# Kernel tuning notes

Hardware: AMD Instinct MI355X
Metric: run time of the kernel (lower is better)

## Reference

```python
import jax, jax.numpy as jnp
import numpy as np
import math

B, S, D, H = 2, 2048, 1024, 16
DH = D // H  # head_dim = 64


def setup_inputs() -> dict:
    key = jax.random.key(0)
    k0, k1, k2 = jax.random.split(key, 3)
    x = jax.random.normal(k0, (B, S, D), dtype=jnp.float32)
    Wi = jax.random.normal(k1, (3 * D, D), dtype=jnp.float32) * 0.02  # torch (out,in) layout
    bi = jnp.zeros((3 * D,), dtype=jnp.float32)
    Wo = jax.random.normal(k2, (D, D), dtype=jnp.float32) * 0.02
    bo = jnp.zeros((D,), dtype=jnp.float32)
    return {"x": x, "Wi": Wi, "bi": bi, "Wo": Wo, "bo": bo, "causal_mask": 1}


def reference(x, Wi, bi, Wo, bo, causal_mask):
    b, s, d = x.shape
    # fused QKV projection: nn.Linear applies x @ W.T + b
    qkv = x @ Wi.T + bi                      # (b, s, 3d)
    q, k, v = jnp.split(qkv, 3, axis=-1)
    # (b, s, d) -> (b, h, s, dh)
    def to_heads(t):
        return t.reshape(b, s, H, DH).transpose(0, 2, 1, 3)
    q, k, v = to_heads(q), to_heads(k), to_heads(v)
    scores = jnp.einsum("bhqd,bhkd->bhqk", q, k)  # (b, h, s, s)
    if causal_mask:
        # mask strictly-upper triangle with -inf BEFORE scaling (as in source; -inf unaffected)
        tri = jnp.triu(jnp.ones((s, s), dtype=bool), k=1)
        scores = jnp.where(tri, -jnp.inf, scores)
    scores = scores / math.sqrt(DH)
    weight = jax.nn.softmax(scores, axis=-1)
    out = jnp.einsum("bhqk,bhkd->bhqd", weight, v)  # (b, h, s, dh)
    out = out.transpose(0, 2, 1, 3).reshape(b, s, d)
    return out @ Wo.T + bo
```

## Files before the change

kernel.cpp:

```cpp
#include <hip/hip_runtime.h>
#include <hip/hip_bf16.h>
#include <stdint.h>

#define B_    2
#define S_    2048
#define D_    1024
#define H_    16
#define DH_   64
#define MTOT  (B_*S_)
#define NQKV  (3*D_)

typedef __attribute__((ext_vector_type(8))) short  bf16x8;
typedef __attribute__((ext_vector_type(4))) short  bf16x4;
typedef __attribute__((ext_vector_type(4))) float  f32x4;
typedef __attribute__((ext_vector_type(8))) unsigned short u16x8;
typedef unsigned short ushort_t;

__device__ __forceinline__ ushort_t f2bf(float f) {
  union { float f; unsigned int i; } v; v.f = f;
  unsigned int r = v.i + 0x7FFF + ((v.i >> 16) & 1);
  return (ushort_t)(r >> 16);
}

__device__ __forceinline__ unsigned cvt_pk_bf16(float lo, float hi) {
  unsigned r;
  asm("v_cvt_pk_bf16_f32 %0, %1, %2" : "=v"(r) : "v"(lo), "v"(hi));
  return r;
}

__device__ __forceinline__ float fexp2(float x) {
  float r;
  asm("v_exp_f32 %0, %1" : "=v"(r) : "v"(x));
  return r;
}

#if __has_builtin(__builtin_amdgcn_mfma_f32_16x16x16_bf16)
__device__ __forceinline__ f32x4 mfma16(bf16x4 a, bf16x4 b, f32x4 c) {
  return __builtin_amdgcn_mfma_f32_16x16x16_bf16(a, b, c, 0, 0, 0);
}
#elif __has_builtin(__builtin_amdgcn_mfma_f32_16x16x16bf16_1k)
__device__ __forceinline__ f32x4 mfma16(bf16x4 a, bf16x4 b, f32x4 c) {
  return __builtin_amdgcn_mfma_f32_16x16x16bf16_1k(a, b, c, 0, 0, 0);
}
#else
__device__ __forceinline__ f32x4 mfma16(bf16x4 a, bf16x4 b, f32x4 c) {
  asm volatile("v_mfma_f32_16x16x16_bf16 %0, %1, %2, %0"
               : "+v"(c) : "v"(a), "v"(b));
  return c;
}
#endif

__device__ __forceinline__ void gl_lds16(const ushort_t* g, ushort_t* l) {
  __builtin_amdgcn_global_load_lds(
      (const __attribute__((address_space(1))) unsigned int*)g,
      (__attribute__((address_space(3))) unsigned int*)l, 16, 0, 0);
}

#define CVN1 (MTOT*D_/8)
#define CVN2 (NQKV*D_/8)
#define CVN3 (D_*D_/8)
__global__ __launch_bounds__(256) void cvt_all(
    const float* __restrict__ x, const float* __restrict__ Wi, const float* __restrict__ Wo,
    ushort_t* __restrict__ xb, ushort_t* __restrict__ Wib, ushort_t* __restrict__ Wob) {
  int i = blockIdx.x * blockDim.x + threadIdx.x;
  const float* src; ushort_t* dst; int k;
  if (i < CVN1)            { src = x;  dst = xb;  k = i; }
  else if (i < CVN1+CVN2)  { src = Wi; dst = Wib; k = i - CVN1; }
  else                     { src = Wo; dst = Wob; k = i - CVN1 - CVN2; }
  const float4* s4 = (const float4*)src;
  float4 a = s4[2*k], b = s4[2*k+1];
  u16x8 o;
  o[0]=f2bf(a.x); o[1]=f2bf(a.y); o[2]=f2bf(a.z); o[3]=f2bf(a.w);
  o[4]=f2bf(b.x); o[5]=f2bf(b.y); o[6]=f2bf(b.z); o[7]=f2bf(b.w);
  ((u16x8*)dst)[k] = o;
}

#define BKQ 32
#define BKO 64
#define QSCALE 0.18033688011112042f
__global__ __launch_bounds__(256) void gemm_qkv(
    const ushort_t* __restrict__ Abf, const ushort_t* __restrict__ Bbf,
    const float* __restrict__ bias,
    ushort_t* __restrict__ qb, ushort_t* __restrict__ kb, ushort_t* __restrict__ vb) {
  __shared__ __align__(16) ushort_t Al[128*BKQ];
  __shared__ __align__(16) ushort_t Bl[128*BKQ];
  int tid = threadIdx.x;
  int w = tid >> 6, lane = tid & 63;
  int wrow = (w >> 1) * 64, wcol = (w & 1) * 64;
  int m0 = blockIdx.y * 128, n0 = blockIdx.x * 128;
  const int K = D_;
  f32x4 zero = {0.f, 0.f, 0.f, 0.f};
  f32x4 acc[4][4];
  for (int i=0;i<4;i++) for (int j=0;j<4;j++) acc[i][j] = zero;

  for (int k0 = 0; k0 < K; k0 += BKQ) {
    __syncthreads();
    for (int it = 0; it < 2; ++it) {
      int c = it*256 + tid;
      int row = c >> 2, cc = c & 3;
      int lbase = (it*256 + w*64) * 8;
      gl_lds16(Abf + (size_t)(m0+row)*K + k0 + cc*8, Al + lbase);
      gl_lds16(Bbf + (size_t)(n0+row)*K + k0 + cc*8, Bl + lbase);
    }
    asm volatile("s_waitcnt vmcnt(0)" ::: "memory");
    __syncthreads();
    int kof = (lane >> 4) * 8;
    bf16x8 af[4], bfr[4];
    for (int i=0;i<4;i++) af[i]  = *(const bf16x8*)(Al + (wrow + i*16 + (lane&15))*BKQ + kof);
    for (int j=0;j<4;j++) bfr[j] = *(const bf16x8*)(Bl + (wcol + j*16 + (lane&15))*BKQ + kof);
    for (int i=0;i<4;i++)
      for (int j=0;j<4;j++)
        acc[i][j] = __builtin_amdgcn_mfma_f32_16x16x32_bf16(af[i], bfr[j], acc[i][j], 0, 0, 0);
  }
  for (int i=0;i<4;i++)
    for (int j=0;j<4;j++)
      for (int r=0;r<4;r++) {
        int gm = m0 + wrow + i*16 + (lane>>4)*4 + r;
        int gn = n0 + wcol + j*16 + (lane&15);
        float v = acc[i][j][r] + bias[gn];
        int b = gm >> 11, s = gm & (S_-1);
        int sect = gn >> 10, hn = gn & (D_-1);
        int hh = hn >> 6, d = hn & 63;
        size_t idx = (((size_t)(b*H_ + hh))*S_ + s)*DH_ + d;
        if (sect == 0) v *= QSCALE;
        ushort_t val = f2bf(v);
        if (sect == 0) qb[idx] = val;
        else if (sect == 1) kb[idx] = val;
        else vb[idx] = val;
      }
}

__global__ __launch_bounds__(256) void transpose_v(
    const ushort_t* __restrict__ vb, ushort_t* __restrict__ vtb) {
  __shared__ ushort_t T[64*72];
  int bh = blockIdx.y;
  int s0 = blockIdx.x * 64;
  int tid = threadIdx.x;
  const ushort_t* src = vb + (size_t)bh * S_ * DH_;
  ushort_t* dst = vtb + (size_t)bh * DH_ * S_;
  for (int it = 0; it < 2; ++it) {
    int c = it*256 + tid;
    int row = c >> 3, cc = c & 7;
    *(uint4*)&T[row*72 + cc*8] = *(const uint4*)(src + (size_t)(s0+row)*DH_ + cc*8);
  }
  __syncthreads();
  for (int it = 0; it < 2; ++it) {
    int c = it*256 + tid;
    int d = c >> 3, sc = c & 7;
    u16x8 o;
    #pragma unroll
    for (int e = 0; e < 8; ++e) o[e] = T[(sc*8+e)*72 + d];
    *(u16x8*)(dst + (size_t)d*S_ + s0 + sc*8) = o;
  }
}

#define KVB 64
#define DTHR 8.0f
__global__ __launch_bounds__(256) void attn_fwd(
    const ushort_t* __restrict__ qb, const ushort_t* __restrict__ kb,
    const ushort_t* __restrict__ vtb, ushort_t* __restrict__ attnb,
    const int* __restrict__ causal) {
  int wg = blockIdx.x;
  int xcd = wg & 7;
  int j = wg >> 3;
  int v = j >> 5;
  int u = j & 31;
  int a = u >> 2;
  int qi = v*8 + ((v & 1) ? (7 - a) : a);
  int qblk = 31 - qi;
  int bh = (u & 3) * 8 + xcd;
  int b = bh >> 4, h = bh & 15;
  int tid = threadIdx.x, w = tid >> 6, lane = tid & 63;
  int g = lane >> 4, q16 = lane & 15;
  const ushort_t* qh  = qb  + (size_t)bh * S_ * DH_;
  const ushort_t* kh  = kb  + (size_t)bh * S_ * DH_;
  const ushort_t* vth = vtb + (size_t)bh * DH_ * S_;
  __shared__ __align__(16) ushort_t Kl[2][KVB*64];
  __shared__ __align__(16) ushort_t Vtl[2][64*KVB];
  bool use_causal = (causal[0] != 0);

  int nkv = use_causal ? (qblk + 1) : (S_/KVB);
  int qw = qblk*64 + w*16;

  bf16x8 qc0 = *(const bf16x8*)(qh + (size_t)(qw + q16)*DH_ +  0 + g*8);
  bf16x8 qc1 = *(const bf16x8*)(qh + (size_t)(qw + q16)*DH_ + 32 + g*8);

  int c0 = tid, c1 = tid + 256;
  int r0 = c0 >> 3, sw0 = ((c0 & 7) ^ (r0 & 7)) * 8;
  int r1 = c1 >> 3, sw1 = ((c1 & 7) ^ (r1 & 7)) * 8;
  const ushort_t* kp0 = kh + r0*DH_ + sw0;
  const ushort_t* kp1 = kh + r1*DH_ + sw1;
  const ushort_t* vp0 = vth + (size_t)r0*S_ + sw0;
  const ushort_t* vp1 = vth + (size_t)r1*S_ + sw1;

  auto stage = [&](int t, int buf) {
    size_t kadv = (size_t)(t*KVB) * DH_;
    int vadv = t*KVB;
    gl_lds16(kp0 + kadv, &Kl[buf][c0*8]);
    gl_lds16(kp1 + kadv, &Kl[buf][c1*8]);
    gl_lds16(vp0 + vadv, &Vtl[buf][c0*8]);
    gl_lds16(vp1 + vadv, &Vtl[buf][c1*8]);
  };

  f32x4 zero = {0.f,0.f,0.f,0.f};
  f32x4 o[4];
  #pragma unroll
  for (int dt=0;dt<4;dt++) o[dt] = zero;
  float mrun = -1e30f, lrun = 0.f;

  stage(0, 0);
  asm volatile("s_waitcnt vmcnt(0)" ::: "memory");
  __builtin_amdgcn_s_barrier();

  for (int it = 0; it < nkv; ++it) {
    int cur = it & 1;
    int kvbase = it * KVB;
    if (it + 1 < nkv) stage(it + 1, cur ^ 1);

    f32x4 sacc[4];
    #pragma unroll
    for (int j2=0;j2<4;j2++) sacc[j2] = zero;
    #pragma unroll
    for (int kk=0;kk<2;kk++) {
      bf16x8 qf = kk ? qc1 : qc0;
      #pragma unroll
      for (int j2=0;j2<4;j2++) {
        int row = j2*16 + q16;
        int slot = (kk*4 + g) ^ (row & 7);
        bf16x8 kf = *(const bf16x8*)(&Kl[cur][row*64 + slot*8]);
        sacc[j2] = __builtin_amdgcn_mfma_f32_16x16x32_bf16(kf, qf, sacc[j2], 0, 0, 0);
      }
    }
    if (use_causal && kvbase + KVB - 1 > qw) {
      int qd = qw + q16 - kvbase;
      #pragma unroll
      for (int j2=0;j2<4;j2++)
        #pragma unroll
        for (int r=0;r<4;r++)
          if (16*j2 + 4*g + r > qd) sacc[j2][r] = -1e30f;
    }
    float m0v = fmaxf(fmaxf(sacc[0][0], sacc[0][1]), fmaxf(sacc[0][2], sacc[0][3]));
    float m1v = fmaxf(fmaxf(sacc[1][0], sacc[1][1]), fmaxf(sacc[1][2], sacc[1][3]));
    float m2v = fmaxf(fmaxf(sacc[2][0], sacc[2][1]), fmaxf(sacc[2][2], sacc[2][3]));
    float m3v = fmaxf(fmaxf(sacc[3][0], sacc[3][1]), fmaxf(sacc[3][2], sacc[3][3]));
    float mx = fmaxf(fmaxf(m0v, m1v), fmaxf(m2v, m3v));
    mx = fmaxf(mx, __shfl_xor(mx, 16, 64));
    mx = fmaxf(mx, __shfl_xor(mx, 32, 64));
    if (!__all(mx - mrun <= DTHR)) {
      float mnew = fmaxf(mrun, mx);
      float alpha = fexp2(mrun - mnew);
      lrun *= alpha;
      float av0 = __shfl(alpha, 4*g + 0, 64);
      float av1 = __shfl(alpha, 4*g + 1, 64);
      float av2 = __shfl(alpha, 4*g + 2, 64);
      float av3 = __shfl(alpha, 4*g + 3, 64);
      #pragma unroll
      for (int dt=0;dt<4;dt++) {
        o[dt][0] *= av0; o[dt][1] *= av1; o[dt][2] *= av2; o[dt][3] *= av3;
      }
      mrun = mnew;
    }
    float p[4][4];
    float rs = 0.f;
    #pragma unroll
    for (int j2=0;j2<4;j2++)
      #pragma unroll
      for (int r=0;r<4;r++) {
        p[j2][r] = fexp2(sacc[j2][r] - mrun);
        rs += p[j2][r];
      }
    rs += __shfl_xor(rs, 16, 64);
    rs += __shfl_xor(rs, 32, 64);
    lrun += rs;
    #pragma unroll
    for (int s=0;s<4;s++) {
      union { unsigned u2[2]; bf16x4 v2; } pk;
      pk.u2[0] = cvt_pk_bf16(p[s][0], p[s][1]);
      pk.u2[1] = cvt_pk_bf16(p[s][2], p[s][3]);
      int E = 16*s + 4*g;
      #pragma unroll
      for (int dt=0;dt<4;dt++) {
        int row = dt*16 + q16;
        int off = row*64 + ((E >> 3) ^ (row & 7))*8 + (E & 7);
        bf16x4 vf = *(const bf16x4*)(&Vtl[cur][off]);
        o[dt] = mfma16(pk.v2, vf, o[dt]);
      }
    }
    asm volatile("s_waitcnt vmcnt(0)" ::: "memory");
    __builtin_amdgcn_s_barrier();
  }
  float li0 = 1.f / __shfl(lrun, 4*g + 0, 64);
  float li1 = 1.f / __shfl(lrun, 4*g + 1, 64);
  float li2 = 1.f / __shfl(lrun, 4*g + 2, 64);
  float li3 = 1.f / __shfl(lrun, 4*g + 3, 64);
  #pragma unroll
  for (int r=0;r<4;r++) {
    float li = (r==0)?li0:(r==1)?li1:(r==2)?li2:li3;
    int q = qw + 4*g + r;
    #pragma unroll
    for (int dt=0;dt<4;dt++) {
      int d = dt*16 + q16;
      attnb[((size_t)(b*S_ + q))*D_ + h*DH_ + d] = f2bf(o[dt][r] * li);
    }
  }
}

__global__ __launch_bounds__(512) void gemm_out(
    const ushort_t* __restrict__ Abf, const ushort_t* __restrict__ Bbf,
    const float* __restrict__ bias, float* __restrict__ out) {
  __shared__ __align__(16) ushort_t Al[128*BKO];
  __shared__ __align__(16) ushort_t Bl[128*BKO];
  int tid = threadIdx.x;
  int w = tid >> 6, lane = tid & 63;
  int g = lane >> 4, q16 = lane & 15;
  int wrow = (w >> 2) * 64, wcol = (w & 3) * 32;
  int m0 = blockIdx.y * 128, n0 = blockIdx.x * 128;
  const int K = D_;
  f32x4 zero = {0.f,0.f,0.f,0.f};
  f32x4 acc[4][2];
  for (int i=0;i<4;i++) for (int j=0;j<2;j++) acc[i][j] = zero;

  for (int k0 = 0; k0 < K; k0 += BKO) {
    __syncthreads();
    #pragma unroll
    for (int it = 0; it < 2; ++it) {
      int c = it*512 + tid;
      int row = c >> 3, scc = ((c & 7) ^ (row & 7)) * 8;
      gl_lds16(Abf + (size_t)(m0+row)*K + k0 + scc, Al + c*8);
      gl_lds16(Bbf + (size_t)(n0+row)*K + k0 + scc, Bl + c*8);
    }
    asm volatile("s_waitcnt vmcnt(0)" ::: "memory");
    __syncthreads();
    #pragma unroll
    for (int kk = 0; kk < 2; ++kk) {
      bf16x8 af[4], bfr[2];
      #pragma unroll
      for (int i=0;i<4;i++) {
        int row = wrow + i*16 + q16;
        int slot = ((kk*4 + g) ^ (row & 7)) * 8;
        af[i] = *(const bf16x8*)(Al + row*BKO + slot);
      }
      #pragma unroll
      for (int j=0;j<2;j++) {
        int row = wcol + j*16 + q16;
        int slot = ((kk*4 + g) ^ (row & 7)) * 8;
        bfr[j] = *(const bf16x8*)(Bl + row*BKO + slot);
      }
      #pragma unroll
      for (int i=0;i<4;i++)
        #pragma unroll
        for (int j=0;j<2;j++)
          acc[i][j] = __builtin_amdgcn_mfma_f32_16x16x32_bf16(af[i], bfr[j], acc[i][j], 0, 0, 0);
    }
  }
  #pragma unroll
  for (int i=0;i<4;i++)
    #pragma unroll
    for (int j=0;j<2;j++)
      #pragma unroll
      for (int r=0;r<4;r++) {
        int gm = m0 + wrow + i*16 + g*4 + r;
        int gn = n0 + wcol + j*16 + q16;
        out[(size_t)gm*D_ + gn] = acc[i][j][r] + bias[gn];
      }
}

extern "C" void kernel_launch(void* const* d_in, const int* in_sizes, int n_in,
                              void* d_out, int out_size, void* d_ws, size_t ws_size,
                              hipStream_t stream) {
  const float* x  = (const float*)d_in[0];
  const float* Wi = (const float*)d_in[1];
  const float* bi = (const float*)d_in[2];
  const float* Wo = (const float*)d_in[3];
  const float* bo = (const float*)d_in[4];
  const int* causal = (const int*)d_in[5];
  float* out = (float*)d_out;

  ushort_t* xb   = (ushort_t*)d_ws;
  ushort_t* Wib  = xb  + (size_t)MTOT*D_;
  ushort_t* Wob  = Wib + (size_t)NQKV*D_;
  ushort_t* qbuf = Wob + (size_t)D_*D_;
  ushort_t* kbuf = qbuf + (size_t)B_*H_*S_*DH_;
  ushort_t* vbuf = kbuf + (size_t)B_*H_*S_*DH_;
  ushort_t* attnb = vbuf + (size_t)B_*H_*S_*DH_;
  ushort_t* vtb  = xb;

  int ntot = CVN1 + CVN2 + CVN3;
  cvt_all<<<(ntot+255)/256, 256, 0, stream>>>(x, Wi, Wo, xb, Wib, Wob);

  gemm_qkv<<<dim3(NQKV/128, MTOT/128), 256, 0, stream>>>(xb, Wib, bi, qbuf, kbuf, vbuf);
  transpose_v<<<dim3(S_/64, B_*H_), 256, 0, stream>>>(vbuf, vtb);
  attn_fwd<<<1024, 256, 0, stream>>>(qbuf, kbuf, vtb, attnb, causal);
  gemm_out<<<dim3(D_/128, MTOT/128), 512, 0, stream>>>(attnb, Wob, bo, out);
}
```

Measured before the change: 120.0 us.

## Double-buffer LDS staging in both GEMMs and swizzle QKV block order

Both projection GEMMs now keep two LDS buffers, so the next K-tile's global-to-LDS loads are issued before the MFMA work on the current tile. This overlaps memory latency with compute and uses one barrier per iteration instead of two. The QKV GEMM also remaps block IDs into a swizzled order to improve L2 reuse of A/B tiles. The cost is twice the LDS, which can lower occupancy, and a reliance on raw s_barrier plus waitcnt for correctness.

```diff
diff --git a/kernel.cpp b/kernel.cpp
--- a/kernel.cpp
+++ b/kernel.cpp
@@ -82,35 +82,49 @@
     const ushort_t* __restrict__ Abf, const ushort_t* __restrict__ Bbf,
     const float* __restrict__ bias,
     ushort_t* __restrict__ qb, ushort_t* __restrict__ kb, ushort_t* __restrict__ vb) {
-  __shared__ __align__(16) ushort_t Al[128*BKQ];
-  __shared__ __align__(16) ushort_t Bl[128*BKQ];
+  __shared__ __align__(16) ushort_t Al[2][128*BKQ];
+  __shared__ __align__(16) ushort_t Bl[2][128*BKQ];
   int tid = threadIdx.x;
   int w = tid >> 6, lane = tid & 63;
   int wrow = (w >> 1) * 64, wcol = (w & 1) * 64;
-  int m0 = blockIdx.y * 128, n0 = blockIdx.x * 128;
+  int bid = blockIdx.y * 24 + blockIdx.x;
+  int swz = (bid & 7) * 96 + (bid >> 3);
+  int m0 = (swz / 24) * 128, n0 = (swz % 24) * 128;
   const int K = D_;
-  f32x4 zero = {0.f, 0.f, 0.f, 0.f};
-  f32x4 acc[4][4];
-  for (int i=0;i<4;i++) for (int j=0;j<4;j++) acc[i][j] = zero;
-
-  for (int k0 = 0; k0 < K; k0 += BKQ) {
-    __syncthreads();
+  const int nt = K / BKQ;
+
+  auto stageg = [&](int t, int buf) {
+    int k0 = t * BKQ;
+    #pragma unroll
     for (int it = 0; it < 2; ++it) {
       int c = it*256 + tid;
       int row = c >> 2, cc = c & 3;
       int lbase = (it*256 + w*64) * 8;
-      gl_lds16(Abf + (size_t)(m0+row)*K + k0 + cc*8, Al + lbase);
-      gl_lds16(Bbf + (size_t)(n0+row)*K + k0 + cc*8, Bl + lbase);
-    }
-    asm volatile("s_waitcnt vmcnt(0)" ::: "memory");
-    __syncthreads();
+      gl_lds16(Abf + (size_t)(m0+row)*K + k0 + cc*8, &Al[buf][lbase]);
+      gl_lds16(Bbf + (size_t)(n0+row)*K + k0 + cc*8, &Bl[buf][lbase]);
+    }
+  };
+
+  f32x4 zero = {0.f, 0.f, 0.f, 0.f};
+  f32x4 acc[4][4];
+  for (int i=0;i<4;i++) for (int j=0;j<4;j++) acc[i][j] = zero;
+
+  stageg(0, 0);
+  asm volatile("s_waitcnt vmcnt(0)" ::: "memory");
+  __builtin_amdgcn_s_barrier();
+
+  for (int t = 0; t < nt; ++t) {
+    int cur = t & 1;
+    if (t + 1 < nt) stageg(t + 1, cur ^ 1);
     int kof = (lane >> 4) * 8;
     bf16x8 af[4], bfr[4];
-    for (int i=0;i<4;i++) af[i]  = *(const bf16x8*)(Al + (wrow + i*16 + (lane&15))*BKQ + kof);
-    for (int j=0;j<4;j++) bfr[j] = *(const bf16x8*)(Bl + (wcol + j*16 + (lane&15))*BKQ + kof);
+    for (int i=0;i<4;i++) af[i]  = *(const bf16x8*)(&Al[cur][(wrow + i*16 + (lane&15))*BKQ + kof]);
+    for (int j=0;j<4;j++) bfr[j] = *(const bf16x8*)(&Bl[cur][(wcol + j*16 + (lane&15))*BKQ + kof]);
     for (int i=0;i<4;i++)
       for (int j=0;j<4;j++)
         acc[i][j] = __builtin_amdgcn_mfma_f32_16x16x32_bf16(af[i], bfr[j], acc[i][j], 0, 0, 0);
+    asm volatile("s_waitcnt vmcnt(0)" ::: "memory");
+    __builtin_amdgcn_s_barrier();
   }
   for (int i=0;i<4;i++)
     for (int j=0;j<4;j++)
@@ -308,29 +322,38 @@
 __global__ __launch_bounds__(512) void gemm_out(
     const ushort_t* __restrict__ Abf, const ushort_t* __restrict__ Bbf,
     const float* __restrict__ bias, float* __restrict__ out) {
-  __shared__ __align__(16) ushort_t Al[128*BKO];
-  __shared__ __align__(16) ushort_t Bl[128*BKO];
+  __shared__ __align__(16) ushort_t Al[2][128*BKO];
+  __shared__ __align__(16) ushort_t Bl[2][128*BKO];
   int tid = threadIdx.x;
   int w = tid >> 6, lane = tid & 63;
   int g = lane >> 4, q16 = lane & 15;
   int wrow = (w >> 2) * 64, wcol = (w & 3) * 32;
   int m0 = blockIdx.y * 128, n0 = blockIdx.x * 128;
   const int K = D_;
+  const int nt = K / BKO;
+
+  auto stageg = [&](int t, int buf) {
+    int k0 = t * BKO;
+    #pragma unroll
+    for (int it = 0; it < 2; ++it) {
+      int c = it*512 + tid;
+      int row = c >> 3, scc = ((c & 7) ^ (row & 7)) * 8;
+      gl_lds16(Abf + (size_t)(m0+row)*K + k0 + scc, &Al[buf][c*8]);
+      gl_lds16(Bbf + (size_t)(n0+row)*K + k0 + scc, &Bl[buf][c*8]);
+    }
+  };
+
   f32x4 zero = {0.f,0.f,0.f,0.f};
   f32x4 acc[4][2];
   for (int i=0;i<4;i++) for (int j=0;j<2;j++) acc[i][j] = zero;
 
-  for (int k0 = 0; k0 < K; k0 += BKO) {
-    __syncthreads();
-    #pragma unroll
-    for (int it = 0; it < 2; ++it) {
-      int c = it*512 + tid;
-      int row = c >> 3, scc = ((c & 7) ^ (row & 7)) * 8;
-      gl_lds16(Abf + (size_t)(m0+row)*K + k0 + scc, Al + c*8);
-      gl_lds16(Bbf + (size_t)(n0+row)*K + k0 + scc, Bl + c*8);
-    }
-    asm volatile("s_waitcnt vmcnt(0)" ::: "memory");
-    __syncthreads();
+  stageg(0, 0);
+  asm volatile("s_waitcnt vmcnt(0)" ::: "memory");
+  __builtin_amdgcn_s_barrier();
+
+  for (int t = 0; t < nt; ++t) {
+    int cur = t & 1;
+    if (t + 1 < nt) stageg(t + 1, cur ^ 1);
     #pragma unroll
     for (int kk = 0; kk < 2; ++kk) {
       bf16x8 af[4], bfr[2];
@@ -338,13 +361,13 @@
       for (int i=0;i<4;i++) {
         int row = wrow + i*16 + q16;
         int slot = ((kk*4 + g) ^ (row & 7)) * 8;
-        af[i] = *(const bf16x8*)(Al + row*BKO + slot);
+        af[i] = *(const bf16x8*)(&Al[cur][row*BKO + slot]);
       }
       #pragma unroll
       for (int j=0;j<2;j++) {
         int row = wcol + j*16 + q16;
         int slot = ((kk*4 + g) ^ (row & 7)) * 8;
-        bfr[j] = *(const bf16x8*)(Bl + row*BKO + slot);
+        bfr[j] = *(const bf16x8*)(&Bl[cur][row*BKO + slot]);
       }
       #pragma unroll
       for (int i=0;i<4;i++)
@@ -352,6 +375,8 @@
         for (int j=0;j<2;j++)
           acc[i][j] = __builtin_amdgcn_mfma_f32_16x16x32_bf16(af[i], bfr[j], acc[i][j], 0, 0, 0);
     }
+    asm volatile("s_waitcnt vmcnt(0)" ::: "memory");
+    __builtin_amdgcn_s_barrier();
   }
   #pragma unroll
   for (int i=0;i<4;i++)
```

Measured after the change: 119.6 us (median of 2 runs). About the same (-0.3%).
